# Optimization experiments

Measured on AMD Instinct MI355X. Metric: run time of the kernel, lower is better.

The kernel has to match this reference:

```python
import jax, jax.numpy as jnp
import numpy as np

SAMPLE_RATE = 44100
MAX_DURATION = 5.0
IR_LEN = int(SAMPLE_RATE * MAX_DURATION)   # 220500 taps (~5 s reverb tail)
AUDIO_LEN = SAMPLE_RATE * 60               # 60 s of mono audio


def setup_inputs() -> dict:
    key = jax.random.key(0)
    k1, k2 = jax.random.split(key)
    audio = jax.random.normal(k1, (1, AUDIO_LEN), dtype=jnp.float32)
    ir = jax.random.normal(k2, (IR_LEN,), dtype=jnp.float32)  # learned impulse response parameter
    return {"audio": audio, "ir": ir}


def _fft_correlate_valid(audio, ir):
    """Valid cross-correlation of (audio zero-padded by M-1) with ir.

    Matches torch: pad audio with M-1 trailing zeros, then conv1d (which is
    cross-correlation) in 'valid' mode -> output length N. Computed via FFT
    (O(N log N)) instead of direct O(N*M) convolution; identical math up to
    floating-point rounding.
    """
    B, N = audio.shape
    M = ir.shape[0]
    full = (N + M - 1) + M - 1          # full linear conv length of padded signal
    nfft = 1 << int(np.ceil(np.log2(full)))
    # trailing zero-pad covers both the explicit M-1 padding and FFT padding
    x = jnp.pad(audio, ((0, 0), (0, nfft - N)))
    k = jnp.pad(ir[::-1], (0, nfft - M))  # flip kernel: conv(x, flip(ir)) == correlate(x, ir)
    y = jnp.fft.irfft(jnp.fft.rfft(x, axis=-1) * jnp.fft.rfft(k), n=nfft, axis=-1)
    # valid cross-correlation region of the padded signal: indices [M-1, M-1+N)
    return jax.lax.dynamic_slice_in_dim(y, M - 1, N, axis=-1)


def reference(audio, ir):
    y = _fft_correlate_valid(audio, ir)       # [1, N]
    return y / jnp.max(jnp.abs(y))            # global max-abs normalization
```

## Files before the change

kernel.cpp:

```cpp
#include <hip/hip_runtime.h>
#include <hip/hip_fp16.h>


#define L_FFT (1 << 20)
#define GSTRIDE 273
#define PSCALE (1.0f / 1048576.0f)
#define NBLK_INV 512

__device__ __forceinline__ float2 h2f(__half2 h) { return __half22float2(h); }
__device__ __forceinline__ __half2 f2h(float2 v) { return __floats2half2_rn(v.x, v.y); }

__device__ __forceinline__ float2 cmul(float2 a, float2 b) {
    return make_float2(a.x * b.x - a.y * b.y, a.x * b.y + a.y * b.x);
}

__device__ __forceinline__ void rad4(float2 a, float2 b, float2 c, float2 d,
                                     float2& o0, float2& o1, float2& o2, float2& o3) {
    float2 apc = make_float2(a.x + c.x, a.y + c.y);
    float2 amc = make_float2(a.x - c.x, a.y - c.y);
    float2 bpd = make_float2(b.x + d.x, b.y + d.y);
    float2 bmd = make_float2(b.x - d.x, b.y - d.y);
    o0 = make_float2(apc.x + bpd.x, apc.y + bpd.y);
    o2 = make_float2(apc.x - bpd.x, apc.y - bpd.y);
    o1 = make_float2(amc.x + bmd.y, amc.y - bmd.x);
    o3 = make_float2(amc.x - bmd.y, amc.y + bmd.x);
}

__device__ __forceinline__ void dft16(float2 x[16]) {
    float2 tt[16];
    rad4(x[0], x[4], x[8],  x[12], tt[0],  tt[1],  tt[2],  tt[3]);
    rad4(x[1], x[5], x[9],  x[13], tt[4],  tt[5],  tt[6],  tt[7]);
    rad4(x[2], x[6], x[10], x[14], tt[8],  tt[9],  tt[10], tt[11]);
    rad4(x[3], x[7], x[11], x[15], tt[12], tt[13], tt[14], tt[15]);
    const float C1 = 0.92387953251128675613f, S1 = 0.38268343236508977173f;
    const float C2 = 0.70710678118654752440f;
    const float2 W1 = make_float2( C1, -S1);
    const float2 W2 = make_float2( C2, -C2);
    const float2 W3 = make_float2( S1, -C1);
    const float2 W6 = make_float2(-C2, -C2);
    const float2 W9 = make_float2(-C1,  S1);
    tt[5]  = cmul(tt[5],  W1);
    tt[6]  = cmul(tt[6],  W2);
    tt[7]  = cmul(tt[7],  W3);
    tt[9]  = cmul(tt[9],  W2);
    tt[10] = make_float2(tt[10].y, -tt[10].x);
    tt[11] = cmul(tt[11], W6);
    tt[13] = cmul(tt[13], W3);
    tt[14] = cmul(tt[14], W6);
    tt[15] = cmul(tt[15], W9);
    rad4(tt[0], tt[4], tt[8],  tt[12], x[0], x[4], x[8],  x[12]);
    rad4(tt[1], tt[5], tt[9],  tt[13], x[1], x[5], x[9],  x[13]);
    rad4(tt[2], tt[6], tt[10], tt[14], x[2], x[6], x[10], x[14]);
    rad4(tt[3], tt[7], tt[11], tt[15], x[3], x[7], x[11], x[15]);
}

__device__ __forceinline__ void fft256_core(float2 x[16], int i, int gi,
                                            float2* lds) {
    dft16(x);
    float sa, ca;
    __sincosf(-6.28318530717958647692f * (float)i * (1.0f / 256.0f), &sa, &ca);
    float2 w1 = make_float2(ca, sa);
    float2 w = w1;
#pragma unroll
    for (int k1 = 1; k1 < 16; ++k1) {
        x[k1] = cmul(x[k1], w);
        w = cmul(w, w1);
    }
    float2* base = lds + gi * GSTRIDE;
#pragma unroll
    for (int k1 = 0; k1 < 16; ++k1) base[i * 17 + k1] = x[k1];
    __syncthreads();
#pragma unroll
    for (int q1 = 0; q1 < 16; ++q1) x[q1] = base[q1 * 17 + i];
    dft16(x);
}

__device__ __forceinline__ void fft4096_block(float2 x[16], int tid, float2* lds) {
    dft16(x);
    float sa, ca;
    __sincosf(-6.28318530717958647692f * (float)tid * (1.0f / 4096.0f), &sa, &ca);
    float2 w1 = make_float2(ca, sa);
    float2 w = w1;
#pragma unroll
    for (int a = 1; a < 16; ++a) { x[a] = cmul(x[a], w); w = cmul(w, w1); }
#pragma unroll
    for (int a = 0; a < 16; ++a) lds[a * GSTRIDE + tid] = x[a];
    __syncthreads();
    int an = tid & 15, i2 = tid >> 4;
#pragma unroll
    for (int q = 0; q < 16; ++q) x[q] = lds[an * GSTRIDE + i2 + 16 * q];
    __syncthreads();
    fft256_core(x, i2, an, lds);
}

__device__ __forceinline__ void fft4096_pair(float2 x[16], float2 h[16], int tid,
                                             float2* LX, float2* LH) {
    dft16(x);
    dft16(h);
    float sa, ca;
    __sincosf(-6.28318530717958647692f * (float)tid * (1.0f / 4096.0f), &sa, &ca);
    float2 w1 = make_float2(ca, sa);
    float2 w = w1;
#pragma unroll
    for (int a = 1; a < 16; ++a) {
        x[a] = cmul(x[a], w);
        h[a] = cmul(h[a], w);
        w = cmul(w, w1);
    }
#pragma unroll
    for (int a = 0; a < 16; ++a) {
        LX[a * GSTRIDE + tid] = x[a];
        LH[a * GSTRIDE + tid] = h[a];
    }
    __syncthreads();
    int an = tid & 15, i2 = tid >> 4;
#pragma unroll
    for (int q = 0; q < 16; ++q) {
        x[q] = LX[an * GSTRIDE + i2 + 16 * q];
        h[q] = LH[an * GSTRIDE + i2 + 16 * q];
    }
    __syncthreads();
    fft256_core(x, i2, an, LX);
    fft256_core(h, i2, an, LH);
}

__global__ void fwd1_pack(const float* __restrict__ audio,
                          const float* __restrict__ ir,
                          __half2* __restrict__ dst, int N, int M, int V) {
    __shared__ float2 lds[16 * GSTRIDE];
    int tid = threadIdx.x;
    int gi = tid & 15, i = tid >> 4;
    int bx = blockIdx.x, slot = blockIdx.y;
    int g = bx * 16 + gi;
    __half2* db = dst + (size_t)slot * L_FFT;

    float2 x[16];
#pragma unroll
    for (int q2 = 0; q2 < 16; ++q2) {
        int idx = g + (i + 16 * q2) * (L_FFT / 256);
        float2 v;
        if (slot == 0) {
            v = make_float2(audio[idx], audio[idx + V]);
        } else if (slot == 1) {
            float a2 = (idx + 2 * V < N) ? audio[idx + 2 * V] : 0.f;
            float a3 = (idx + 3 * V < N) ? audio[idx + 3 * V] : 0.f;
            v = make_float2(a2, a3);
        } else {
            v = make_float2((idx < M) ? ir[idx] : 0.f, 0.f);
        }
        x[q2] = v;
    }
    fft256_core(x, i, gi, lds);
    float sa, ca;
    float base = -6.28318530717958647692f * (float)g * (1.0f / (float)L_FFT);
    __sincosf(base * (float)i, &sa, &ca);
    float2 w = make_float2(ca, sa);
    __sincosf(base * 16.0f, &sa, &ca);
    float2 w16 = make_float2(ca, sa);
#pragma unroll
    for (int q = 0; q < 16; ++q) {
        db[(size_t)4096 * (i + 16 * q) + g] = f2h(cmul(x[q], w));
        w = cmul(w, w16);
    }
}

__global__ __launch_bounds__(256, 2) void fused_mid(const __half2* __restrict__ Y1,
                                                    __half2* __restrict__ Mp,
                                                    unsigned* __restrict__ sync) {
    __shared__ float2 LX[16 * GSTRIDE];
    __shared__ float2 LH[16 * GSTRIDE];
    int tid = threadIdx.x;
    int b0 = blockIdx.x, p = blockIdx.y;
    if (b0 == 0 && p == 0 && tid == 0) {
        sync[0] = 0u;
        sync[1] = 0u;
        sync[32] = 0u;
    }
    const __half2* xr = Y1 + (size_t)p * L_FFT + (size_t)4096 * b0;
    const __half2* hr = Y1 + (size_t)2 * L_FFT + (size_t)4096 * b0;
    float2 x[16], h[16];
#pragma unroll
    for (int w = 0; w < 16; ++w) {
        x[w] = h2f(xr[tid + 256 * w]);
        h[w] = h2f(hr[tid + 256 * w]);
    }
    fft4096_pair(x, h, tid, LX, LH);
#pragma unroll
    for (int r = 0; r < 16; ++r) {
        float2 Z = x[r], H = h[r];
        x[r] = make_float2((Z.x * H.x + Z.y * H.y) * PSCALE,
                           (Z.x * H.y - Z.y * H.x) * PSCALE);
    }
    fft4096_block(x, tid, LX);
    float sa, ca;
    float base = -6.28318530717958647692f * (float)b0 * (1.0f / (float)L_FFT);
    __sincosf(base * (float)tid, &sa, &ca);
    float2 w = make_float2(ca, sa);
    __sincosf(base * 256.0f, &sa, &ca);
    float2 ws = make_float2(ca, sa);
    __half2* dst = Mp + (size_t)p * L_FFT + (size_t)4096 * b0;
#pragma unroll
    for (int r = 0; r < 16; ++r) {
        dst[tid + 256 * r] = f2h(cmul(x[r], w));
        w = cmul(w, ws);
    }
}

__global__ __launch_bounds__(256, 2) void inv_norm_write(
        const __half2* __restrict__ Mp, float* __restrict__ out,
        unsigned* __restrict__ sync, int N, int V) {
    __shared__ float2 lds[16 * GSTRIDE];
    __shared__ float sm[4];
    __shared__ float bcast;
    int tid = threadIdx.x;
    int gi = tid & 15, i = tid >> 4;
    int bx = blockIdx.x, p = blockIdx.y;
    const __half2* sb = Mp + (size_t)p * L_FFT;
    int na = 16 * bx + gi;
    float2 x[16];
#pragma unroll
    for (int q = 0; q < 16; ++q)
        x[q] = h2f(sb[(size_t)4096 * (i + 16 * q) + na]);
    fft256_core(x, i, gi, lds);
    int nbase = na + 4096 * i;
    int lenO = (p == 1) ? (N - 3 * V) : V;
    float m = 0.f;
#pragma unroll
    for (int r = 0; r < 16; ++r) {
        int n = nbase + r * 65536;
        if (n < V)    m = fmaxf(m, fabsf(x[r].x));
        if (n < lenO) m = fmaxf(m, fabsf(x[r].y));
    }
    for (int o = 32; o > 0; o >>= 1) m = fmaxf(m, __shfl_xor(m, o));
    int lane = tid & 63, wv = tid >> 6;
    if (lane == 0) sm[wv] = m;
    __syncthreads();
    if (tid == 0) {
        float bm = fmaxf(fmaxf(sm[0], sm[1]), fmaxf(sm[2], sm[3]));
        atomicMax(&sync[0], __float_as_uint(bm));
        unsigned old = __hip_atomic_fetch_add(&sync[1], 1u, __ATOMIC_ACQ_REL,
                                              __HIP_MEMORY_SCOPE_AGENT);
        unsigned v;
        if (old == NBLK_INV - 1) {
            v = __hip_atomic_load(&sync[0], __ATOMIC_ACQUIRE,
                                  __HIP_MEMORY_SCOPE_AGENT);
            __hip_atomic_store(&sync[32], v, __ATOMIC_RELEASE,
                               __HIP_MEMORY_SCOPE_AGENT);
        } else {
            for (;;) {
                v = __hip_atomic_load(&sync[32], __ATOMIC_ACQUIRE,
                                      __HIP_MEMORY_SCOPE_AGENT);
                if (v != 0u) break;
                __builtin_amdgcn_s_sleep(32);
                if (__hip_atomic_load(&sync[1], __ATOMIC_ACQUIRE,
                                      __HIP_MEMORY_SCOPE_AGENT) >= NBLK_INV) {
                    v = __hip_atomic_load(&sync[0], __ATOMIC_ACQUIRE,
                                          __HIP_MEMORY_SCOPE_AGENT);
                    break;
                }
            }
        }
        bcast = __uint_as_float(v);
    }
    __syncthreads();
    float inv = 1.0f / bcast;
    int se = 2 * p, so = 2 * p + 1;
#pragma unroll
    for (int r = 0; r < 16; ++r) {
        int n = nbase + r * 65536;
        if (n < V)    out[(size_t)se * V + n] = x[r].x * inv;
        if (n < lenO) out[(size_t)so * V + n] = -x[r].y * inv;
    }
}

extern "C" void kernel_launch(void* const* d_in, const int* in_sizes, int n_in,
                              void* d_out, int out_size, void* d_ws, size_t ws_size,
                              hipStream_t stream) {
    const float* audio = (const float*)d_in[0];
    const float* ir    = (const float*)d_in[1];
    float* out = (float*)d_out;

    const int N = in_sizes[0];
    const int M = in_sizes[1];
    const int V = L_FFT - M + 1;

    __half2* A = (__half2*)d_ws;
    __half2* B = A + (size_t)3 * L_FFT;
    unsigned* sync = (unsigned*)(B + (size_t)3 * L_FFT);

    fwd1_pack<<<dim3(256, 3), 256, 0, stream>>>(audio, ir, B, N, M, V);
    fused_mid<<<dim3(256, 2), 256, 0, stream>>>(B, A, sync);
    inv_norm_write<<<dim3(256, 2), 256, 0, stream>>>(A, out, sync, N, V);
}
```

Measured before the change: 121.0 us.

## Use hierarchical two-level grid barrier with per-group counters and publish lines

Replaces the single global atomic max/counter grid barrier in the inverse FFT kernel with a two-level scheme. Blocks reduce into one of 16 cache-line-separated group counters, the last block of each group forwards to a global counter, and the final one publishes the max to 16 separate lines that each group spins on. The aim is to cut atomic contention and polling traffic on one hot cache line, at the cost of extra atomics on the critical path and more sync-line initialisation.

```diff
diff --git a/kernel.cpp b/kernel.cpp
--- a/kernel.cpp
+++ b/kernel.cpp
@@ -6,6 +6,11 @@
 #define GSTRIDE 273
 #define PSCALE (1.0f / 1048576.0f)
 #define NBLK_INV 512
+#define NGRP 16
+#define GRPSZ (NBLK_INV / NGRP)
+#define GLOB_LINE 16
+#define PUB_LINE 17
+#define SYNC_LINES 33
 
 __device__ __forceinline__ float2 h2f(__half2 h) { return __half22float2(h); }
 __device__ __forceinline__ __half2 f2h(float2 v) { return __floats2half2_rn(v.x, v.y); }
@@ -171,10 +176,9 @@
     __shared__ float2 LH[16 * GSTRIDE];
     int tid = threadIdx.x;
     int b0 = blockIdx.x, p = blockIdx.y;
-    if (b0 == 0 && p == 0 && tid == 0) {
-        sync[0] = 0u;
-        sync[1] = 0u;
-        sync[32] = 0u;
+    if (b0 == 0 && p == 0 && tid < SYNC_LINES) {
+        sync[tid * 32 + 0] = 0u;
+        sync[tid * 32 + 1] = 0u;
     }
     const __half2* xr = Y1 + (size_t)p * L_FFT + (size_t)4096 * b0;
     const __half2* hr = Y1 + (size_t)2 * L_FFT + (size_t)4096 * b0;
@@ -237,27 +241,40 @@
     __syncthreads();
     if (tid == 0) {
         float bm = fmaxf(fmaxf(sm[0], sm[1]), fmaxf(sm[2], sm[3]));
-        atomicMax(&sync[0], __float_as_uint(bm));
-        unsigned old = __hip_atomic_fetch_add(&sync[1], 1u, __ATOMIC_ACQ_REL,
+        int lb = (p << 8) | bx;
+        int grp = lb & (NGRP - 1);
+        unsigned* gl = sync + grp * 32;
+        unsigned* gg = sync + GLOB_LINE * 32;
+        unsigned* pub = sync + (PUB_LINE + grp) * 32;
+        atomicMax(&gl[0], __float_as_uint(bm));
+        unsigned old = __hip_atomic_fetch_add(&gl[1], 1u, __ATOMIC_ACQ_REL,
                                               __HIP_MEMORY_SCOPE_AGENT);
+        if (old == GRPSZ - 1) {
+            unsigned gm = __hip_atomic_load(&gl[0], __ATOMIC_ACQUIRE,
+                                            __HIP_MEMORY_SCOPE_AGENT);
+            atomicMax(&gg[0], gm);
+            unsigned gold = __hip_atomic_fetch_add(&gg[1], 1u, __ATOMIC_ACQ_REL,
+                                                   __HIP_MEMORY_SCOPE_AGENT);
+            if (gold == NGRP - 1) {
+                unsigned total = __hip_atomic_load(&gg[0], __ATOMIC_ACQUIRE,
+                                                   __HIP_MEMORY_SCOPE_AGENT);
+#pragma unroll
+                for (int k = 0; k < NGRP; ++k)
+                    __hip_atomic_store(sync + (PUB_LINE + k) * 32, total,
+                                       __ATOMIC_RELEASE, __HIP_MEMORY_SCOPE_AGENT);
+            }
+        }
         unsigned v;
-        if (old == NBLK_INV - 1) {
-            v = __hip_atomic_load(&sync[0], __ATOMIC_ACQUIRE,
+        for (;;) {
+            v = __hip_atomic_load(pub, __ATOMIC_ACQUIRE,
                                   __HIP_MEMORY_SCOPE_AGENT);
-            __hip_atomic_store(&sync[32], v, __ATOMIC_RELEASE,
-                               __HIP_MEMORY_SCOPE_AGENT);
-        } else {
-            for (;;) {
-                v = __hip_atomic_load(&sync[32], __ATOMIC_ACQUIRE,
+            if (v != 0u) break;
+            __builtin_amdgcn_s_sleep(32);
+            if (__hip_atomic_load(&gg[1], __ATOMIC_ACQUIRE,
+                                  __HIP_MEMORY_SCOPE_AGENT) >= NGRP) {
+                v = __hip_atomic_load(&gg[0], __ATOMIC_ACQUIRE,
                                       __HIP_MEMORY_SCOPE_AGENT);
-                if (v != 0u) break;
-                __builtin_amdgcn_s_sleep(32);
-                if (__hip_atomic_load(&sync[1], __ATOMIC_ACQUIRE,
-                                      __HIP_MEMORY_SCOPE_AGENT) >= NBLK_INV) {
-                    v = __hip_atomic_load(&sync[0], __ATOMIC_ACQUIRE,
-                                          __HIP_MEMORY_SCOPE_AGENT);
-                    break;
-                }
+                break;
             }
         }
         bcast = __uint_as_float(v);
```

Result: slower. 133.5 us (+10.3%).
